# Kernel tuning notes

Hardware: AMD Instinct MI355X
Metric: run time of the kernel (lower is better)

Reference implementation:

```python
import jax, jax.numpy as jnp
import numpy as np


def _lstm(x, k, r, b, return_sequences=True):
    # Keras LSTM: gate order i, f, c(g), o; sigmoid recurrent activation, tanh activation.
    # x: [B,T,D], k: [D,4H], r: [H,4H], b: [4H]
    B = x.shape[0]
    H = r.shape[0]
    xk = jnp.einsum('btd,dh->bth', x, k) + b  # precompute input projections for all steps

    def step(carry, xk_t):
        h, c = carry
        z = xk_t + h @ r
        i, f, g, o = jnp.split(z, 4, axis=-1)
        i = jax.nn.sigmoid(i)
        f = jax.nn.sigmoid(f)
        g = jnp.tanh(g)
        o = jax.nn.sigmoid(o)
        c = f * c + i * g
        h = o * jnp.tanh(c)
        return (h, c), h

    h0 = jnp.zeros((B, H), x.dtype)
    (hT, _), hs = jax.lax.scan(step, (h0, jnp.zeros_like(h0)), jnp.swapaxes(xk, 0, 1))
    if return_sequences:
        return jnp.swapaxes(hs, 0, 1)  # [B,T,H]
    return hT  # [B,H]


def _bias(h):
    # Keras unit_forget_bias=True: forget-gate bias initialized to 1
    return jnp.zeros((4 * h,), jnp.float32).at[h:2 * h].set(1.0)


def setup_inputs() -> dict:
    key = jax.random.key(0)
    ks = jax.random.split(key, 20)
    B, T, D = 128, 512, 64
    s = 0.05

    def n(k, shape):
        return jax.random.normal(k, shape, jnp.float32) * s

    inp = {"x": jax.random.normal(ks[0], (B, T, D), jnp.float32)}
    lstm_dims = [(D, 640), (640, 400), (400, 256), (256, 256)]
    i = 1
    for li, (din, h) in enumerate(lstm_dims, 1):
        inp[f"k{li}"] = n(ks[i], (din, 4 * h))
        inp[f"r{li}"] = n(ks[i + 1], (h, 4 * h))
        inp[f"b{li}"] = _bias(h)
        i += 2
    dense_dims = [(256, 512), (512, 256), (256, 128), (128, 64), (64, 16), (16, 3)]
    for li, (din, dout) in enumerate(dense_dims, 1):
        inp[f"wd{li}"] = n(ks[i], (din, dout))
        inp[f"bd{li}"] = jnp.zeros((dout,), jnp.float32)
        i += 1
    return inp


def reference(x, k1, r1, b1, k2, r2, b2, k3, r3, b3, k4, r4, b4,
              wd1, bd1, wd2, bd2, wd3, bd3, wd4, bd4, wd5, bd5, wd6, bd6):
    h = _lstm(x, k1, r1, b1, return_sequences=True)
    h = _lstm(h, k2, r2, b2, return_sequences=True)
    h = _lstm(h, k3, r3, b3, return_sequences=True)
    h = _lstm(h, k4, r4, b4, return_sequences=False)  # [B, 256]
    # Dropout layers are identity at inference (Keras call without training=True)
    h = jax.nn.relu(h @ wd1 + bd1)
    h = jax.nn.relu(h @ wd2 + bd2)
    h = jax.nn.relu(h @ wd3 + bd3)
    h = jax.nn.relu(h @ wd4 + bd4)
    h = jax.nn.relu(h @ wd5 + bd5)
    logits = h @ wd6 + bd6
    return jax.nn.softmax(logits, axis=-1)  # class_count=3 branch
```

## Files before the change

kernel.cpp:

```cpp
#include <hip/hip_runtime.h>
#include <hip/hip_cooperative_groups.h>
#include <cstdint>
#include <cstddef>

namespace cg = cooperative_groups;

typedef _Float16 f16;
typedef _Float16 h8v  __attribute__((ext_vector_type(8)));
typedef float    f32x4 __attribute__((ext_vector_type(4)));

static constexpr int BATCH  = 128;
static constexpr int TSTEPS = 512;
static constexpr int NT     = 256;

static constexpr int TB1 = 80, TB2 = 100, TB3 = 32, TB4 = 32;
static constexpr int TNB   = TB1 + TB2 + TB3 + TB4;
static constexpr int NGRID = TNB + 4;

template<int RING> struct WS {
  static constexpr size_t XT  = 0;
  static constexpr size_t H1  = XT + 512ull * 128 * 64 * 2;
  static constexpr size_t H2  = H1 + (size_t)RING * 128 * 640 * 2 + 64;
  static constexpr size_t H3  = H2 + (size_t)RING * 128 * 400 * 2 + 64;
  static constexpr size_t H4  = H3 + (size_t)RING * 128 * 256 * 2 + 64;
  static constexpr size_t PK1 = H4 + (size_t)RING * 128 * 256 * 2 + 64;
  static constexpr size_t PK2 = PK1 + (size_t)TB1 * 32 * 704  * 2;
  static constexpr size_t PK3 = PK2 + (size_t)TB2 * 16 * 1056 * 2;
  static constexpr size_t PK4 = PK3 + (size_t)TB3 * 32 * 672  * 2;
  static constexpr size_t BAR = PK4 + (size_t)TB4 * 32 * 512  * 2;
  static constexpr size_t ZERO= BAR + 8192;
  static constexpr size_t END = ZERO + 163840;
};

struct KParams {
  const float *x;
  const float *k1, *r1, *b1, *k2, *r2, *b2, *k3, *r3, *b3, *k4, *r4, *b4;
  const float *wd1, *bd1, *wd2, *bd2, *wd3, *bd3, *wd4, *bd4, *wd5, *bd5, *wd6, *bd6;
  float *out;
  char *ws;
};

__device__ __forceinline__ float sigm(float v) { return 1.f / (1.f + expf(-v)); }

__device__ __forceinline__ uint64_t c_load8(const void* p) {
  return __hip_atomic_load((const uint64_t*)p, __ATOMIC_RELAXED, __HIP_MEMORY_SCOPE_AGENT);
}
__device__ __forceinline__ void c_store2(void* p, unsigned short v) {
  __hip_atomic_store((unsigned short*)p, v, __ATOMIC_RELAXED, __HIP_MEMORY_SCOPE_AGENT);
}
__device__ __forceinline__ unsigned short c_load2(const void* p) {
  return __hip_atomic_load((const unsigned short*)p, __ATOMIC_RELAXED, __HIP_MEMORY_SCOPE_AGENT);
}
__device__ __forceinline__ unsigned u_load(const unsigned* p) {
  return __hip_atomic_load(p, __ATOMIC_RELAXED, __HIP_MEMORY_SCOPE_AGENT);
}
__device__ __forceinline__ void u_store(unsigned* p, unsigned v) {
  __hip_atomic_store(p, v, __ATOMIC_RELAXED, __HIP_MEMORY_SCOPE_AGENT);
}
__device__ __forceinline__ void acq_fence() {
  __builtin_amdgcn_fence(__ATOMIC_ACQUIRE, "agent");
}

template<int NBLK>
__device__ void control_role(unsigned* U, int first, int lidx) {
  const int tid = threadIdx.x;
  int cand = 1;
  while (cand <= TSTEPS) {
    unsigned v = (tid < NBLK) ? u_load(&U[first + tid]) : 0xFFFFFFFFu;
    if (__syncthreads_and((int)(v >= (unsigned)cand))) {
      if (tid < 16) u_store(&U[512 + tid * 64 + lidx], (unsigned)cand);
      ++cand;
    }
  }
}

__device__ void prepack_layer(const float* __restrict__ gk, const float* __restrict__ gr,
                              f16* __restrict__ pack, int DIN, int H, int NJ, int KPAD,
                              int TB, int gtid, int gstr) {
  const int KREAL = DIN + H;
  const int NGC = 4 * NJ;
  const long total = (long)TB * NGC * KPAD;
  for (long e = gtid; e < total; e += gstr) {
    const int  k   = (int)(e % KPAD);
    const long r   = e / KPAD;
    const int  n   = (int)(r % NGC);
    const int  blk = (int)(r / NGC);
    const int  g   = n / NJ, jj = n % NJ;
    const int  j   = blk * NJ + jj;
    float v = 0.f;
    if (k < DIN)        v = gk[(size_t)k * 4 * H + (size_t)g * H + j];
    else if (k < KREAL) v = gr[(size_t)(k - DIN) * 4 * H + (size_t)g * H + j];
    pack[e] = (f16)v;
  }
}

#define FETCH(PP, CC) do { \
  _Pragma("unroll") \
  for (int ii_ = 0; ii_ < C; ++ii_) { \
    const int ks_ = (CC) * C + ii_; \
    if (ks_ < KS) { \
      const int k_ = ks_ * 32 + kg; \
      _Pragma("unroll") \
      for (int m_ = 0; m_ < 2; ++m_) { \
        const int bmv_ = m_ ? bm1 : bm0; \
        uint4 v_ = make_uint4(0u, 0u, 0u, 0u); \
        if constexpr (SEQM) { \
          if (k_ < DIN)        v_ = *(const uint4*)(inP + (size_t)bmv_ * DIN + k_); \
          else if (k_ < KREAL) v_ = *(const uint4*)(inH + (size_t)bmv_ * H + (k_ - DIN)); \
        } else { \
          if (k_ < DIN) { \
            const f16* p_ = inP + (size_t)bmv_ * DIN + k_; \
            if constexpr (SEQIN) { \
              ((uint64_t*)&v_)[0] = *(const uint64_t*)p_; \
              ((uint64_t*)&v_)[1] = *(const uint64_t*)(p_ + 4); \
            } else { \
              ((uint64_t*)&v_)[0] = c_load8(p_); \
              ((uint64_t*)&v_)[1] = c_load8(p_ + 4); \
            } \
          } else if (k_ < KREAL) { \
            const f16* p_ = inH + (size_t)bmv_ * H + (k_ - DIN); \
            ((uint64_t*)&v_)[0] = c_load8(p_); \
            ((uint64_t*)&v_)[1] = c_load8(p_ + 4); \
          } \
        } \
        ab[PP][ii_][m_] = v_; \
      } \
    } \
  } \
} while (0)

#define COMPUTE(PP, CC) do { \
  _Pragma("unroll") \
  for (int ii_ = 0; ii_ < C; ++ii_) { \
    const int ks_ = (CC) * C + ii_; \
    if (ks_ < KS) { \
      const int kb_ = ks_ * 32; \
      h8v bf_[NTI]; \
      _Pragma("unroll") \
      for (int nt_ = 0; nt_ < NTI; ++nt_) \
        bf_[nt_] = *(const h8v*)(wlds + (size_t)(nt_ * 16 + l15) * WROW + kb_ + kg); \
      _Pragma("unroll") \
      for (int m_ = 0; m_ < 2; ++m_) { \
        union { uint4 u; h8v v; } af_; \
        af_.u = ab[PP][ii_][m_]; \
        _Pragma("unroll") \
        for (int nt_ = 0; nt_ < NTI; ++nt_) \
          acc[m_][nt_] = __builtin_amdgcn_mfma_f32_16x16x32_f16(af_.v, bf_[nt_], acc[m_][nt_], 0, 0, 0); \
      } \
    } \
  } \
} while (0)

template<int DIN, int H, int NJ, int LIDX, bool SEQIN, int RING>
__device__ void lstm_role(int blk, int bid, const f16* lo_base, f16* ownH,
                          const f16* pack, const float* __restrict__ gbias,
                          const f16* zreg, char* smem, unsigned* U) {
  constexpr bool SEQM = (RING == TSTEPS);
  constexpr int KREAL = DIN + H;
  constexpr int KS    = (KREAL + 31) / 32;
  constexpr int KPAD  = KS * 32;
  constexpr int NGC   = 4 * NJ;
  constexpr int NTI   = NGC / 16;
  constexpr int WROW  = KPAD + 8;
  constexpr int ZROW  = 132;
  constexpr int C     = 6;
  constexpr int NC    = (KS + C - 1) / C;
  static_assert(NC <= 6, "NC");
  static_assert(NGC % 16 == 0 && (DIN % 8) == 0 && (KREAL % 8) == 0, "geom");

  const int tid  = threadIdx.x;
  const int w    = tid >> 6, lane = tid & 63;
  const int l15  = lane & 15;
  const int kg   = (lane >> 4) * 8;
  const int bm0  = w * 32 + l15;
  const int bm1  = bm0 + 16;

  f16*   wlds = (f16*)smem;
  float* z    = (float*)(smem + (size_t)NGC * WROW * 2);

  {
    const f16* src = pack + (size_t)blk * NGC * KPAD;
    constexpr int RU = KPAD / 8;
    for (int u = tid; u < NGC * RU; u += NT) {
      const int n = u / RU, k8 = u % RU;
      *(uint4*)(wlds + (size_t)n * WROW + k8 * 8) =
          *(const uint4*)(src + (size_t)n * KPAD + k8 * 8);
    }
  }
  __syncthreads();

  const int jj = tid >> 5, bg = tid & 31, b0e = bg * 4;
  const bool epi = (tid < NJ * 32);
  const int j = blk * NJ + (epi ? jj : 0);
  const float4 bias = make_float4(gbias[j], gbias[H + j], gbias[2 * H + j], gbias[3 * H + j]);
  float cst[4] = {0.f, 0.f, 0.f, 0.f};

  const unsigned* relp = &U[512 + (bid & 15) * 64];
  int rcI = 0, rcO = 0, rcD = 0;
  (void)rcI; (void)rcD;

  for (int t = 0; t < TSTEPS; ++t) {
    if (tid == 0) {
      for (;;) {
        bool ok = (rcO >= t);
        if constexpr (LIDX > 0) ok = ok && (rcI >= t + 1);
        if constexpr (!SEQM && LIDX < 3) ok = ok && (rcD >= t - (RING - 1));
        if (ok) break;
        if constexpr (LIDX > 0) rcI = (int)u_load(&relp[LIDX - 1]);
        rcO = (int)u_load(&relp[LIDX]);
        if constexpr (!SEQM && LIDX < 3) rcD = (int)u_load(&relp[LIDX + 1]);
      }
    }
    __syncthreads();

    const f16* inP = SEQIN ? lo_base + (size_t)t * DIN * BATCH
                           : lo_base + (size_t)(t & (RING - 1)) * DIN * BATCH;
    const f16* inH = (t == 0) ? zreg
                              : ownH + (size_t)((t - 1) & (RING - 1)) * H * BATCH;

    f32x4 acc[2][NTI];
    {
      const f32x4 zz = {0.f, 0.f, 0.f, 0.f};
      #pragma unroll
      for (int m_ = 0; m_ < 2; ++m_)
        #pragma unroll
        for (int nt_ = 0; nt_ < NTI; ++nt_) acc[m_][nt_] = zz;
    }

    uint4 ab[3][C][2];

    FETCH(0, 0);
    if constexpr (NC > 1) FETCH(1, 1);
    if constexpr (NC > 2) FETCH(2, 2);
    COMPUTE(0, 0);
    if constexpr (NC > 1) { if constexpr (NC > 3) FETCH(0, 3); COMPUTE(1, 1); }
    if constexpr (NC > 2) { if constexpr (NC > 4) FETCH(1, 4); COMPUTE(2, 2); }
    if constexpr (NC > 3) { if constexpr (NC > 5) FETCH(2, 5); COMPUTE(0, 3); }
    if constexpr (NC > 4) COMPUTE(1, 4);
    if constexpr (NC > 5) COMPUTE(2, 5);

    #pragma unroll
    for (int m_ = 0; m_ < 2; ++m_)
      #pragma unroll
      for (int nt_ = 0; nt_ < NTI; ++nt_)
        *(f32x4*)(z + (size_t)(nt_ * 16 + l15) * ZROW + w * 32 + m_ * 16 + (lane >> 4) * 4) =
            acc[m_][nt_];
    __syncthreads();

    if (epi) {
      const float* zb = z + b0e;
      const f32x4 zi = *(const f32x4*)(zb + (size_t)(0 * NJ + jj) * ZROW);
      const f32x4 zf = *(const f32x4*)(zb + (size_t)(1 * NJ + jj) * ZROW);
      const f32x4 zg = *(const f32x4*)(zb + (size_t)(2 * NJ + jj) * ZROW);
      const f32x4 zo = *(const f32x4*)(zb + (size_t)(3 * NJ + jj) * ZROW);
      f16* dst = ownH + (size_t)(t & (RING - 1)) * H * BATCH + j;
      #pragma unroll
      for (int q = 0; q < 4; ++q) {
        const float ig = sigm(zi[q] + bias.x);
        const float fg = sigm(zf[q] + bias.y);
        const float gg = tanhf(zg[q] + bias.z);
        const float og = sigm(zo[q] + bias.w);
        cst[q] = fg * cst[q] + ig * gg;
        const float hv = og * tanhf(cst[q]);
        union { f16 h; unsigned short u; } o2; o2.h = (f16)hv;
        c_store2(dst + (size_t)(b0e + q) * H, o2.u);
      }
    }
    asm volatile("s_waitcnt vmcnt(0)" ::: "memory");
    __syncthreads();
    if (tid == 0) u_store(&U[bid], (unsigned)(t + 1));
  }
}
#undef FETCH
#undef COMPUTE

__device__ void dense_stage(const float* in, float* outb,
                            const float* __restrict__ w, const float* __restrict__ bias,
                            int din, int dout, bool relu) {
  for (int jc = threadIdx.x; jc < dout; jc += NT) {
    float s = bias[jc];
    for (int d = 0; d < din; ++d) s += in[d] * w[(size_t)d * dout + jc];
    outb[jc] = relu ? fmaxf(s, 0.f) : s;
  }
  __syncthreads();
}

constexpr size_t cmax(size_t a, size_t b) { return a > b ? a : b; }
constexpr size_t wlz(int NGC, int KPAD) {
  return (size_t)NGC * (KPAD + 8) * 2 + (size_t)NGC * 132 * 4;
}
static constexpr size_t SMEM_BYTES =
    cmax(cmax(wlz(32, 704), wlz(16, 1056)),
         cmax(cmax(wlz(32, 672), wlz(32, 512)), (size_t)4096));
static_assert(SMEM_BYTES <= 65536, "LDS");

template<int RING>
__global__ __launch_bounds__(NT, 1) void fused_kernel(KParams p) {
  using L = WS<RING>;
  cg::grid_group grid = cg::this_grid();
  __shared__ __attribute__((aligned(16))) char smem[SMEM_BYTES];

  char* ws = p.ws;
  unsigned* U = (unsigned*)(ws + L::BAR);
  const f16* zreg = (const f16*)(ws + L::ZERO);
  const int tid  = threadIdx.x;
  const int bid  = blockIdx.x;
  const int gtid = bid * NT + tid;
  const int gstr = NGRID * NT;

  prepack_layer(p.k1, p.r1, (f16*)(ws + L::PK1), 64,  640, 8, 704,  TB1, gtid, gstr);
  prepack_layer(p.k2, p.r2, (f16*)(ws + L::PK2), 640, 400, 4, 1056, TB2, gtid, gstr);
  prepack_layer(p.k3, p.r3, (f16*)(ws + L::PK3), 400, 256, 8, 672,  TB3, gtid, gstr);
  prepack_layer(p.k4, p.r4, (f16*)(ws + L::PK4), 256, 256, 8, 512,  TB4, gtid, gstr);

  {
    f16* xT = (f16*)(ws + L::XT);
    const long total = (long)TSTEPS * BATCH * 8;
    for (long u = gtid; u < total; u += gstr) {
      const int  d8 = (int)(u & 7);
      const long r  = u >> 3;
      const int  b  = (int)(r & (BATCH - 1));
      const int  t  = (int)(r >> 7);
      const float* src = p.x + ((size_t)b * TSTEPS + t) * 64 + d8 * 8;
      const float4 v0 = *(const float4*)src;
      const float4 v1 = *(const float4*)(src + 4);
      h8v o;
      o[0] = (f16)v0.x; o[1] = (f16)v0.y; o[2] = (f16)v0.z; o[3] = (f16)v0.w;
      o[4] = (f16)v1.x; o[5] = (f16)v1.y; o[6] = (f16)v1.z; o[7] = (f16)v1.w;
      *(h8v*)(xT + ((size_t)t * BATCH + b) * 64 + d8 * 8) = o;
    }
  }

  grid.sync();
  acq_fence();

  constexpr int TRB2 = TB1, TRB3 = TB1 + TB2, TRB4 = TB1 + TB2 + TB3;
  if (bid >= TNB) {
    const int l = bid - TNB;
    if (l == 0)      control_role<TB1>(U, 0,    0);
    else if (l == 1) control_role<TB2>(U, TRB2, 1);
    else if (l == 2) control_role<TB3>(U, TRB3, 2);
    else             control_role<TB4>(U, TRB4, 3);
  } else if (bid < TRB2) {
    lstm_role< 64, 640, 8, 0, true , RING>(bid, bid, (const f16*)(ws + L::XT),
        (f16*)(ws + L::H1), (const f16*)(ws + L::PK1), p.b1, zreg, smem, U);
  } else if (bid < TRB3) {
    lstm_role<640, 400, 4, 1, false, RING>(bid - TRB2, bid, (const f16*)(ws + L::H1),
        (f16*)(ws + L::H2), (const f16*)(ws + L::PK2), p.b2, zreg, smem, U);
  } else if (bid < TRB4) {
    lstm_role<400, 256, 8, 2, false, RING>(bid - TRB3, bid, (const f16*)(ws + L::H2),
        (f16*)(ws + L::H3), (const f16*)(ws + L::PK3), p.b3, zreg, smem, U);
  } else {
    lstm_role<256, 256, 8, 3, false, RING>(bid - TRB4, bid, (const f16*)(ws + L::H3),
        (f16*)(ws + L::H4), (const f16*)(ws + L::PK4), p.b4, zreg, smem, U);
  }

  if (bid < BATCH) {
    if (tid == 0) {
      const unsigned* relp = &U[512 + (bid & 15) * 64];
      while ((int)u_load(&relp[3]) < TSTEPS) {}
    }
    __syncthreads();
    const int b = bid;
    float* A = (float*)smem;
    float* B = (float*)smem + 512;
    const f16* h4 = (const f16*)(ws + L::H4)
                  + (size_t)((TSTEPS - 1) & (RING - 1)) * 256 * BATCH + (size_t)b * 256;
    for (int d = tid; d < 256; d += NT) {
      union { unsigned short u; f16 h; } cc;
      cc.u = c_load2(h4 + d);
      A[d] = (float)cc.h;
    }
    __syncthreads();
    dense_stage(A, B, p.wd1, p.bd1, 256, 512, true);
    dense_stage(B, A, p.wd2, p.bd2, 512, 256, true);
    dense_stage(A, B, p.wd3, p.bd3, 256, 128, true);
    dense_stage(B, A, p.wd4, p.bd4, 128, 64,  true);
    dense_stage(A, B, p.wd5, p.bd5, 64,  16,  true);
    dense_stage(B, A, p.wd6, p.bd6, 16,  3,   false);
    if (tid == 0) {
      float z0 = A[0], z1 = A[1], z2 = A[2];
      float m  = fmaxf(fmaxf(z0, z1), z2);
      float e0 = expf(z0 - m), e1 = expf(z1 - m), e2 = expf(z2 - m);
      float s  = e0 + e1 + e2;
      p.out[b * 3 + 0] = e0 / s;
      p.out[b * 3 + 1] = e1 / s;
      p.out[b * 3 + 2] = e2 / s;
    }
  }
}

extern "C" void kernel_launch(void* const* d_in, const int* in_sizes, int n_in,
                              void* d_out, int out_size, void* d_ws, size_t ws_size,
                              hipStream_t stream) {
  (void)in_sizes; (void)n_in; (void)out_size;
  KParams prm;
  prm.x  = (const float*)d_in[0];
  prm.k1 = (const float*)d_in[1];  prm.r1 = (const float*)d_in[2];  prm.b1 = (const float*)d_in[3];
  prm.k2 = (const float*)d_in[4];  prm.r2 = (const float*)d_in[5];  prm.b2 = (const float*)d_in[6];
  prm.k3 = (const float*)d_in[7];  prm.r3 = (const float*)d_in[8];  prm.b3 = (const float*)d_in[9];
  prm.k4 = (const float*)d_in[10]; prm.r4 = (const float*)d_in[11]; prm.b4 = (const float*)d_in[12];
  prm.wd1 = (const float*)d_in[13]; prm.bd1 = (const float*)d_in[14];
  prm.wd2 = (const float*)d_in[15]; prm.bd2 = (const float*)d_in[16];
  prm.wd3 = (const float*)d_in[17]; prm.bd3 = (const float*)d_in[18];
  prm.wd4 = (const float*)d_in[19]; prm.bd4 = (const float*)d_in[20];
  prm.wd5 = (const float*)d_in[21]; prm.bd5 = (const float*)d_in[22];
  prm.wd6 = (const float*)d_in[23]; prm.bd6 = (const float*)d_in[24];
  prm.out = (float*)d_out;
  prm.ws  = (char*)d_ws;

  const bool big = ws_size >= WS<TSTEPS>::END;
  const size_t bar_off = big ? WS<TSTEPS>::BAR : WS<4>::BAR;
  hipMemsetAsync((char*)d_ws + bar_off, 0, 8192 + 163840, stream);

  void* args[] = { &prm };
  if (big) {
    hipLaunchCooperativeKernel((void*)fused_kernel<TSTEPS>, dim3(NGRID), dim3(NT),
                               args, 0, stream);
  } else {
    hipLaunchCooperativeKernel((void*)fused_kernel<4>, dim3(NGRID), dim3(NT),
                               args, 0, stream);
  }
}
```

Measured before the change: 5.558 ms.

## Replace controller blocks with per-timestep atomic arrival counters for inter-layer sync

Result: slower. 6.378 ms (+14.8%).

```diff
diff --git a/kernel.cpp b/kernel.cpp
--- a/kernel.cpp
+++ b/kernel.cpp
@@ -15,7 +15,7 @@
 
 static constexpr int TB1 = 80, TB2 = 100, TB3 = 32, TB4 = 32;
 static constexpr int TNB   = TB1 + TB2 + TB3 + TB4;
-static constexpr int NGRID = TNB + 4;
+static constexpr int NGRID = TNB;
 
 template<int RING> struct WS {
   static constexpr size_t XT  = 0;
@@ -54,24 +54,11 @@
 __device__ __forceinline__ unsigned u_load(const unsigned* p) {
   return __hip_atomic_load(p, __ATOMIC_RELAXED, __HIP_MEMORY_SCOPE_AGENT);
 }
-__device__ __forceinline__ void u_store(unsigned* p, unsigned v) {
-  __hip_atomic_store(p, v, __ATOMIC_RELAXED, __HIP_MEMORY_SCOPE_AGENT);
+__device__ __forceinline__ void cnt_add(unsigned* p) {
+  (void)__hip_atomic_fetch_add(p, 1u, __ATOMIC_RELAXED, __HIP_MEMORY_SCOPE_AGENT);
 }
 __device__ __forceinline__ void acq_fence() {
   __builtin_amdgcn_fence(__ATOMIC_ACQUIRE, "agent");
-}
-
-template<int NBLK>
-__device__ void control_role(unsigned* U, int first, int lidx) {
-  const int tid = threadIdx.x;
-  int cand = 1;
-  while (cand <= TSTEPS) {
-    unsigned v = (tid < NBLK) ? u_load(&U[first + tid]) : 0xFFFFFFFFu;
-    if (__syncthreads_and((int)(v >= (unsigned)cand))) {
-      if (tid < 16) u_store(&U[512 + tid * 64 + lidx], (unsigned)cand);
-      ++cand;
-    }
-  }
 }
 
 __device__ void prepack_layer(const float* __restrict__ gk, const float* __restrict__ gr,
@@ -152,9 +139,12 @@
 } while (0)
 
 template<int DIN, int H, int NJ, int LIDX, bool SEQIN, int RING>
-__device__ void lstm_role(int blk, int bid, const f16* lo_base, f16* ownH,
+__device__ void lstm_role(int blk, const f16* lo_base, f16* ownH,
                           const f16* pack, const float* __restrict__ gbias,
-                          const f16* zreg, char* smem, unsigned* U) {
+                          const f16* zreg, char* smem,
+                          const unsigned* cntPrev, unsigned tbPrev,
+                          unsigned* cntOwn, unsigned tbOwn,
+                          const unsigned* cntNext, unsigned tbNext) {
   constexpr bool SEQM = (RING == TSTEPS);
   constexpr int KREAL = DIN + H;
   constexpr int KS    = (KREAL + 31) / 32;
@@ -195,20 +185,22 @@
   const float4 bias = make_float4(gbias[j], gbias[H + j], gbias[2 * H + j], gbias[3 * H + j]);
   float cst[4] = {0.f, 0.f, 0.f, 0.f};
 
-  const unsigned* relp = &U[512 + (bid & 15) * 64];
-  int rcI = 0, rcO = 0, rcD = 0;
-  (void)rcI; (void)rcD;
-
   for (int t = 0; t < TSTEPS; ++t) {
-    if (tid == 0) {
-      for (;;) {
-        bool ok = (rcO >= t);
-        if constexpr (LIDX > 0) ok = ok && (rcI >= t + 1);
-        if constexpr (!SEQM && LIDX < 3) ok = ok && (rcD >= t - (RING - 1));
-        if (ok) break;
-        if constexpr (LIDX > 0) rcI = (int)u_load(&relp[LIDX - 1]);
-        rcO = (int)u_load(&relp[LIDX]);
-        if constexpr (!SEQM && LIDX < 3) rcD = (int)u_load(&relp[LIDX + 1]);
+    if (tid < 64) {
+      const unsigned* pp = nullptr; unsigned tgt = 0;
+      if constexpr (LIDX > 0) {
+        if (tid == 0) { pp = cntPrev + t; tgt = tbPrev; }
+      }
+      if (tid == 1 && t > 0) { pp = cntOwn + (t - 1); tgt = tbOwn; }
+      if constexpr (!SEQM && LIDX < 3) {
+        if (tid == 2 && t >= RING) { pp = cntNext + (t - RING); tgt = tbNext; }
+      }
+      bool c = (pp == nullptr);
+      while (!__all((int)c)) {
+        if (!c) {
+          c = (u_load(pp) >= tgt);
+          if (!c) __builtin_amdgcn_s_sleep(8);
+        }
       }
     }
     __syncthreads();
@@ -268,7 +260,7 @@
     }
     asm volatile("s_waitcnt vmcnt(0)" ::: "memory");
     __syncthreads();
-    if (tid == 0) u_store(&U[bid], (unsigned)(t + 1));
+    if (tid == 0) cnt_add(cntOwn + t);
   }
 }
 #undef FETCH
@@ -301,7 +293,7 @@
   __shared__ __attribute__((aligned(16))) char smem[SMEM_BYTES];
 
   char* ws = p.ws;
-  unsigned* U = (unsigned*)(ws + L::BAR);
+  unsigned* cnt = (unsigned*)(ws + L::BAR);
   const f16* zreg = (const f16*)(ws + L::ZERO);
   const int tid  = threadIdx.x;
   const int bid  = blockIdx.x;
@@ -335,30 +327,33 @@
   acq_fence();
 
   constexpr int TRB2 = TB1, TRB3 = TB1 + TB2, TRB4 = TB1 + TB2 + TB3;
-  if (bid >= TNB) {
-    const int l = bid - TNB;
-    if (l == 0)      control_role<TB1>(U, 0,    0);
-    else if (l == 1) control_role<TB2>(U, TRB2, 1);
-    else if (l == 2) control_role<TB3>(U, TRB3, 2);
-    else             control_role<TB4>(U, TRB4, 3);
-  } else if (bid < TRB2) {
-    lstm_role< 64, 640, 8, 0, true , RING>(bid, bid, (const f16*)(ws + L::XT),
-        (f16*)(ws + L::H1), (const f16*)(ws + L::PK1), p.b1, zreg, smem, U);
+  if (bid < TRB2) {
+    lstm_role< 64, 640, 8, 0, true , RING>(bid, (const f16*)(ws + L::XT),
+        (f16*)(ws + L::H1), (const f16*)(ws + L::PK1), p.b1, zreg, smem,
+        nullptr, 0u, cnt + 0 * 512, (unsigned)TB1, cnt + 1 * 512, (unsigned)TB2);
   } else if (bid < TRB3) {
-    lstm_role<640, 400, 4, 1, false, RING>(bid - TRB2, bid, (const f16*)(ws + L::H1),
-        (f16*)(ws + L::H2), (const f16*)(ws + L::PK2), p.b2, zreg, smem, U);
+    lstm_role<640, 400, 4, 1, false, RING>(bid - TRB2, (const f16*)(ws + L::H1),
+        (f16*)(ws + L::H2), (const f16*)(ws + L::PK2), p.b2, zreg, smem,
+        cnt + 0 * 512, (unsigned)TB1, cnt + 1 * 512, (unsigned)TB2, cnt + 2 * 512, (unsigned)TB3);
   } else if (bid < TRB4) {
-    lstm_role<400, 256, 8, 2, false, RING>(bid - TRB3, bid, (const f16*)(ws + L::H2),
-        (f16*)(ws + L::H3), (const f16*)(ws + L::PK3), p.b3, zreg, smem, U);
+    lstm_role<400, 256, 8, 2, false, RING>(bid - TRB3, (const f16*)(ws + L::H2),
+        (f16*)(ws + L::H3), (const f16*)(ws + L::PK3), p.b3, zreg, smem,
+        cnt + 1 * 512, (unsigned)TB2, cnt + 2 * 512, (unsigned)TB3, cnt + 3 * 512, (unsigned)TB4);
   } else {
-    lstm_role<256, 256, 8, 3, false, RING>(bid - TRB4, bid, (const f16*)(ws + L::H3),
-        (f16*)(ws + L::H4), (const f16*)(ws + L::PK4), p.b4, zreg, smem, U);
+    lstm_role<256, 256, 8, 3, false, RING>(bid - TRB4, (const f16*)(ws + L::H3),
+        (f16*)(ws + L::H4), (const f16*)(ws + L::PK4), p.b4, zreg, smem,
+        cnt + 2 * 512, (unsigned)TB3, cnt + 3 * 512, (unsigned)TB4, nullptr, 0u);
   }
 
   if (bid < BATCH) {
-    if (tid == 0) {
-      const unsigned* relp = &U[512 + (bid & 15) * 64];
-      while ((int)u_load(&relp[3]) < TSTEPS) {}
+    if (tid < 64) {
+      bool c = (tid != 0);
+      while (!__all((int)c)) {
+        if (!c) {
+          c = (u_load(cnt + 3 * 512 + TSTEPS - 1) >= (unsigned)TB4);
+          if (!c) __builtin_amdgcn_s_sleep(8);
+        }
+      }
     }
     __syncthreads();
     const int b = bid;
```

## Defer own-layer wait past input-projection chunks and vectorize h stores

Applied to the files above, without the earlier changes.

Result: faster. 5.003 ms (-10.0%).

```diff
diff --git a/kernel.cpp b/kernel.cpp
--- a/kernel.cpp
+++ b/kernel.cpp
@@ -45,8 +45,8 @@
 __device__ __forceinline__ uint64_t c_load8(const void* p) {
   return __hip_atomic_load((const uint64_t*)p, __ATOMIC_RELAXED, __HIP_MEMORY_SCOPE_AGENT);
 }
-__device__ __forceinline__ void c_store2(void* p, unsigned short v) {
-  __hip_atomic_store((unsigned short*)p, v, __ATOMIC_RELAXED, __HIP_MEMORY_SCOPE_AGENT);
+__device__ __forceinline__ void c_store8(void* p, uint64_t v) {
+  __hip_atomic_store((uint64_t*)p, v, __ATOMIC_RELAXED, __HIP_MEMORY_SCOPE_AGENT);
 }
 __device__ __forceinline__ unsigned short c_load2(const void* p) {
   return __hip_atomic_load((const unsigned short*)p, __ATOMIC_RELAXED, __HIP_MEMORY_SCOPE_AGENT);
@@ -151,6 +151,11 @@
   } \
 } while (0)
 
+#define WAITOWN do { \
+  if (tid == 0) { while (rcO < t) rcO = (int)u_load(&relp[LIDX]); } \
+  __syncthreads(); \
+} while (0)
+
 template<int DIN, int H, int NJ, int LIDX, bool SEQIN, int RING>
 __device__ void lstm_role(int blk, int bid, const f16* lo_base, f16* ownH,
                           const f16* pack, const float* __restrict__ gbias,
@@ -165,7 +170,10 @@
   constexpr int ZROW  = 132;
   constexpr int C     = 6;
   constexpr int NC    = (KS + C - 1) / C;
+  constexpr int KSX   = DIN / 32;
+  constexpr int CH    = KSX / C;
   static_assert(NC <= 6, "NC");
+  static_assert(CH <= NC - 1, "CH");
   static_assert(NGC % 16 == 0 && (DIN % 8) == 0 && (KREAL % 8) == 0, "geom");
 
   const int tid  = threadIdx.x;
@@ -189,10 +197,16 @@
   }
   __syncthreads();
 
-  const int jj = tid >> 5, bg = tid & 31, b0e = bg * 4;
-  const bool epi = (tid < NJ * 32);
-  const int j = blk * NJ + (epi ? jj : 0);
-  const float4 bias = make_float4(gbias[j], gbias[H + j], gbias[2 * H + j], gbias[3 * H + j]);
+  constexpr int JG = NJ / 4;
+  const int be  = tid / JG;
+  const int g4  = tid % JG;
+  const bool epi = (tid < 128 * JG);
+  const int j0  = blk * NJ + g4 * 4;
+  f32x4 bias4[4] = {};
+  if (epi) {
+    #pragma unroll
+    for (int g = 0; g < 4; ++g) bias4[g] = *(const f32x4*)(gbias + (size_t)g * H + j0);
+  }
   float cst[4] = {0.f, 0.f, 0.f, 0.f};
 
   const unsigned* relp = &U[512 + (bid & 15) * 64];
@@ -202,12 +216,13 @@
   for (int t = 0; t < TSTEPS; ++t) {
     if (tid == 0) {
       for (;;) {
-        bool ok = (rcO >= t);
+        bool ok = true;
+        if constexpr (CH == 0) ok = (rcO >= t);
         if constexpr (LIDX > 0) ok = ok && (rcI >= t + 1);
         if constexpr (!SEQM && LIDX < 3) ok = ok && (rcD >= t - (RING - 1));
         if (ok) break;
         if constexpr (LIDX > 0) rcI = (int)u_load(&relp[LIDX - 1]);
-        rcO = (int)u_load(&relp[LIDX]);
+        if constexpr (CH == 0) rcO = (int)u_load(&relp[LIDX]);
         if constexpr (!SEQM && LIDX < 3) rcD = (int)u_load(&relp[LIDX + 1]);
       }
     }
@@ -230,12 +245,12 @@
     uint4 ab[3][C][2];
 
     FETCH(0, 0);
-    if constexpr (NC > 1) FETCH(1, 1);
-    if constexpr (NC > 2) FETCH(2, 2);
+    if constexpr (NC > 1) { if constexpr (CH == 1) WAITOWN; FETCH(1, 1); }
+    if constexpr (NC > 2) { if constexpr (CH == 2) WAITOWN; FETCH(2, 2); }
     COMPUTE(0, 0);
-    if constexpr (NC > 1) { if constexpr (NC > 3) FETCH(0, 3); COMPUTE(1, 1); }
-    if constexpr (NC > 2) { if constexpr (NC > 4) FETCH(1, 4); COMPUTE(2, 2); }
-    if constexpr (NC > 3) { if constexpr (NC > 5) FETCH(2, 5); COMPUTE(0, 3); }
+    if constexpr (NC > 1) { if constexpr (NC > 3) { if constexpr (CH == 3) WAITOWN; FETCH(0, 3); } COMPUTE(1, 1); }
+    if constexpr (NC > 2) { if constexpr (NC > 4) { if constexpr (CH == 4) WAITOWN; FETCH(1, 4); } COMPUTE(2, 2); }
+    if constexpr (NC > 3) { if constexpr (NC > 5) { if constexpr (CH == 5) WAITOWN; FETCH(2, 5); } COMPUTE(0, 3); }
     if constexpr (NC > 4) COMPUTE(1, 4);
     if constexpr (NC > 5) COMPUTE(2, 5);
 
@@ -248,23 +263,26 @@
     __syncthreads();
 
     if (epi) {
-      const float* zb = z + b0e;
-      const f32x4 zi = *(const f32x4*)(zb + (size_t)(0 * NJ + jj) * ZROW);
-      const f32x4 zf = *(const f32x4*)(zb + (size_t)(1 * NJ + jj) * ZROW);
-      const f32x4 zg = *(const f32x4*)(zb + (size_t)(2 * NJ + jj) * ZROW);
-      const f32x4 zo = *(const f32x4*)(zb + (size_t)(3 * NJ + jj) * ZROW);
-      f16* dst = ownH + (size_t)(t & (RING - 1)) * H * BATCH + j;
+      float vi[4], vf[4], vg[4], vo[4];
       #pragma unroll
       for (int q = 0; q < 4; ++q) {
-        const float ig = sigm(zi[q] + bias.x);
-        const float fg = sigm(zf[q] + bias.y);
-        const float gg = tanhf(zg[q] + bias.z);
-        const float og = sigm(zo[q] + bias.w);
+        const int nn = g4 * 4 + q;
+        vi[q] = z[(size_t)(0 * NJ + nn) * ZROW + be];
+        vf[q] = z[(size_t)(1 * NJ + nn) * ZROW + be];
+        vg[q] = z[(size_t)(2 * NJ + nn) * ZROW + be];
+        vo[q] = z[(size_t)(3 * NJ + nn) * ZROW + be];
+      }
+      union { f16 h[4]; uint64_t u; } o;
+      #pragma unroll
+      for (int q = 0; q < 4; ++q) {
+        const float ig = sigm(vi[q] + bias4[0][q]);
+        const float fg = sigm(vf[q] + bias4[1][q]);
+        const float gg = tanhf(vg[q] + bias4[2][q]);
+        const float og = sigm(vo[q] + bias4[3][q]);
         cst[q] = fg * cst[q] + ig * gg;
-        const float hv = og * tanhf(cst[q]);
-        union { f16 h; unsigned short u; } o2; o2.h = (f16)hv;
-        c_store2(dst + (size_t)(b0e + q) * H, o2.u);
+        o.h[q] = (f16)(og * tanhf(cst[q]));
       }
+      c_store8(ownH + (size_t)(t & (RING - 1)) * H * BATCH + (size_t)be * H + j0, o.u);
     }
     asm volatile("s_waitcnt vmcnt(0)" ::: "memory");
     __syncthreads();
@@ -273,6 +291,7 @@
 }
 #undef FETCH
 #undef COMPUTE
+#undef WAITOWN
 
 __device__ void dense_stage(const float* in, float* outb,
                             const float* __restrict__ w, const float* __restrict__ bias,
```
